# Kernel tuning notes

Measured on AMD Instinct MI355X. Metric: run time of the kernel, lower is better.

The kernel has to match this reference:

```python
import jax, jax.numpy as jnp
import numpy as np

B, DV, W, H = 64, 2048, 14, 14
DQ, DA, G, DH, NC = 2400, 1200, 2, 1200, 3000


def setup_inputs() -> dict:
    key = jax.random.key(0)
    ks = jax.random.split(key, 14)
    s = lambda k, shp, scale=0.02: jax.random.normal(k, shp, dtype=jnp.float32) * scale
    return {
        "input_q": jax.random.normal(ks[0], (B, DQ), dtype=jnp.float32),
        "input_v": jax.random.normal(ks[1], (B, DV, W, H), dtype=jnp.float32),
        "Wv_att": s(ks[2], (DA, DV)),
        "bv_att": s(ks[3], (DA,)),
        "Wq_att": s(ks[4], (DA, DQ)),
        "bq_att": s(ks[5], (DA,)),
        "Watt": s(ks[6], (G, DA)),
        "batt": s(ks[7], (G,)),
        "Wv_fus": s(ks[8], (G, DH, DV)),
        "bv_fus": s(ks[9], (G, DH)),
        "Wq_fus": s(ks[10], (G * DH, DQ)),
        "bq_fus": s(ks[11], (G * DH,)),
        "Wc": s(ks[12], (NC, G * DH)),
        "bc": s(ks[13], (NC,)),
    }


def reference(input_q, input_v, Wv_att, bv_att, Wq_att, bq_att, Watt, batt,
              Wv_fus, bv_fus, Wq_fus, bq_fus, Wc, bc):
    b, dv, w, h = input_v.shape
    n = w * h  # spatial positions

    # --- attention branch (eval mode: dropout = identity) ---
    # 1x1 conv == per-position linear over channels; activation_v = tanh
    xv = jnp.tanh(jnp.einsum('bchw,dc->bdhw', input_v, Wv_att) + bv_att[None, :, None, None])
    xv = xv.reshape(b, -1, n).transpose(0, 2, 1)               # [B, WH, DA]
    # question projection; activation_q = tanh
    xq = jnp.tanh(input_q @ Wq_att.T + bq_att)                 # [B, DA]
    # MLB Hadamard fusion + activation_mm = tanh
    xatt = jnp.tanh(xv * xq[:, None, :])                       # [B, WH, DA]
    # glimpse scores: 1x1 conv over dim_mm channels
    wgt = jnp.einsum('bnd,gd->bgn', xatt, Watt) + batt[None, :, None]  # [B, G, WH]
    att = jax.nn.softmax(wgt, axis=-1)                         # softmax over WH per glimpse

    # weighted sum of ORIGINAL features per glimpse
    v_flat = input_v.reshape(b, dv, n)                         # [B, DV, WH]
    v_att = jnp.einsum('bgn,bdn->bgd', att, v_flat)            # [B, G, DV]

    # --- glimpse fusion + classification ---
    v_fus = jnp.tanh(jnp.einsum('bgd,ghd->bgh', v_att, Wv_fus) + bv_fus)  # [B, G, DH]
    v_fus = v_fus.reshape(b, -1)                               # [B, G*DH] (concat over glimpses)
    q_fus = jnp.tanh(input_q @ Wq_fus.T + bq_fus)              # [B, G*DH]
    x = (v_fus * q_fus) @ Wc.T + bc                            # [B, NC]
    return (x, wgt)
```

## Files before the change

kernel.cpp:

```cpp
#include <hip/hip_runtime.h>
#include <hip/hip_fp16.h>

typedef _Float16 half8 __attribute__((ext_vector_type(8)));
typedef float f32x4 __attribute__((ext_vector_type(4)));

__device__ __forceinline__ float tanh_fast(float x) {
  float e = __expf(2.0f * x);
  return 1.0f - 2.0f / (e + 1.0f);
}

__device__ __forceinline__ void gload16(const _Float16* g, _Float16* l) {
  __builtin_amdgcn_global_load_lds((const __attribute__((address_space(1))) void*)g,
                                   (__attribute__((address_space(3))) void*)l,
                                   16, 0, 0);
}

__global__ __launch_bounds__(256) void k_transpose_v(const float* __restrict__ in,
                                                     _Float16* __restrict__ out) {
  __shared__ float t[64][65];
  int b = blockIdx.z;
  int c0 = blockIdx.y * 64;
  int p0 = blockIdx.x * 64;
  int tid = threadIdx.x;
  int pl = tid & 63;
  #pragma unroll
  for (int s = 0; s < 16; ++s) {
    int cl = (tid >> 6) + s * 4;
    int p = p0 + pl;
    t[cl][pl] = (p < 196) ? in[((size_t)b * 2048 + (c0 + cl)) * 196 + p] : 0.0f;
  }
  __syncthreads();
  int c8 = (tid & 7) * 8;
  #pragma unroll
  for (int s = 0; s < 2; ++s) {
    int p = p0 + (tid >> 3) + s * 32;
    if (p < 196) {
      half8 v;
      #pragma unroll
      for (int j = 0; j < 8; ++j) v[j] = (_Float16)t[c8 + j][(tid >> 3) + s * 32];
      *(half8*)(out + ((size_t)b * 196 + p) * 2048 + c0 + c8) = v;
    }
  }
}

__global__ __launch_bounds__(256) void k_prep(const float* __restrict__ W,
                                              _Float16* __restrict__ Wh,
                                              const float* __restrict__ batt,
                                              float* __restrict__ wgt) {
  int i = blockIdx.x * 256 + threadIdx.x;
  int n = i >> 11;
  Wh[i] = (n < 1200) ? (_Float16)W[i] : (_Float16)0.0f;
  if (i < 25088) wgt[i] = batt[(i / 196) & 1];
}

__global__ __launch_bounds__(256) void k_gemm1(const _Float16* __restrict__ A,
                                               const _Float16* __restrict__ B,
                                               const float* __restrict__ bias,
                                               const float* __restrict__ xq,
                                               const float* __restrict__ Watt,
                                               float* __restrict__ wgt) {
  __shared__ __align__(16) _Float16 As[2][128 * 32];
  __shared__ __align__(16) _Float16 Bs[2][128 * 32];
  int tid = threadIdx.x;
  int n0 = blockIdx.x * 128;
  int m0 = blockIdx.y * 128;
  int lane = tid & 63;
  int wave = tid >> 6;
  int wm = (wave >> 1) * 64;
  int wn = (wave & 1) * 64;
  int fr = lane & 15;
  int fq = lane >> 4;

  int rl = lane >> 2;
  int cch = lane & 3;
  int row0 = wave * 32 + rl;
  int row1 = wave * 32 + 16 + rl;
  int g0 = cch ^ ((row0 >> 1) & 3);
  int g1 = cch ^ ((row1 >> 1) & 3);
  const _Float16* aSrc0 = A + (size_t)(m0 + row0) * 2048 + g0 * 8;
  const _Float16* aSrc1 = A + (size_t)(m0 + row1) * 2048 + g1 * 8;
  const _Float16* bSrc0 = B + (size_t)(n0 + row0) * 2048 + g0 * 8;
  const _Float16* bSrc1 = B + (size_t)(n0 + row1) * 2048 + g1 * 8;

  f32x4 acc[4][4];
  #pragma unroll
  for (int i = 0; i < 4; ++i)
    #pragma unroll
    for (int j = 0; j < 4; ++j) acc[i][j] = (f32x4){0.f, 0.f, 0.f, 0.f};

  auto stage = [&](int buf, int k0) {
    _Float16* dA = &As[buf][(wave * 32) * 32];
    _Float16* dB = &Bs[buf][(wave * 32) * 32];
    gload16(aSrc0 + k0, dA);
    gload16(aSrc1 + k0, dA + 16 * 32);
    gload16(bSrc0 + k0, dB);
    gload16(bSrc1 + k0, dB + 16 * 32);
  };
  int sw = (fr >> 1) & 3;
  auto compute = [&](int buf) {
    half8 af[4], bf[4];
    #pragma unroll
    for (int mt = 0; mt < 4; ++mt)
      af[mt] = *(const half8*)(&As[buf][(wm + mt * 16 + fr) * 32 + ((fq ^ sw) << 3)]);
    #pragma unroll
    for (int nt = 0; nt < 4; ++nt)
      bf[nt] = *(const half8*)(&Bs[buf][(wn + nt * 16 + fr) * 32 + ((fq ^ sw) << 3)]);
    #pragma unroll
    for (int mt = 0; mt < 4; ++mt)
      #pragma unroll
      for (int nt = 0; nt < 4; ++nt)
        acc[mt][nt] = __builtin_amdgcn_mfma_f32_16x16x32_f16(af[mt], bf[nt], acc[mt][nt], 0, 0, 0);
  };

  stage(0, 0);
  stage(1, 32);
  for (int kt = 0; kt < 63; ++kt) {
    int cur = kt & 1;
    asm volatile("s_waitcnt vmcnt(4)" ::: "memory");
    __builtin_amdgcn_s_barrier();
    compute(cur);
    asm volatile("s_waitcnt lgkmcnt(0)" ::: "memory");
    __builtin_amdgcn_s_barrier();
    if (kt < 62) stage(cur, (kt + 2) * 32);
  }
  asm volatile("s_waitcnt vmcnt(0)" ::: "memory");
  __builtin_amdgcn_s_barrier();
  compute(1);

  float s0[16], s1[16];
  #pragma unroll
  for (int i = 0; i < 16; ++i) { s0[i] = 0.f; s1[i] = 0.f; }

  #pragma unroll
  for (int nt = 0; nt < 4; ++nt) {
    int col = n0 + wn + nt * 16 + fr;
    bool ok = col < 1200;
    float bcol = ok ? bias[col] : 0.f;
    float wa0 = ok ? Watt[col] : 0.f;
    float wa1 = ok ? Watt[1200 + col] : 0.f;
    #pragma unroll
    for (int mt = 0; mt < 4; ++mt) {
      #pragma unroll
      for (int r = 0; r < 4; ++r) {
        int row = m0 + wm + mt * 16 + fq * 4 + r;
        int b = row / 196;
        float xqv = ok ? xq[b * 1200 + col] : 0.f;
        float xv = tanh_fast(acc[mt][nt][r] + bcol);
        float xa = tanh_fast(xv * xqv);
        s0[mt * 4 + r] += xa * wa0;
        s1[mt * 4 + r] += xa * wa1;
      }
    }
  }
  #pragma unroll
  for (int i = 0; i < 16; ++i) {
    #pragma unroll
    for (int off = 8; off > 0; off >>= 1) {
      s0[i] += __shfl_down(s0[i], off);
      s1[i] += __shfl_down(s1[i], off);
    }
  }
  if (fr == 0) {
    #pragma unroll
    for (int i = 0; i < 16; ++i) {
      int row = m0 + wm + (i >> 2) * 16 + fq * 4 + (i & 3);
      int b = row / 196;
      int p = row - b * 196;
      atomicAdd(&wgt[(b * 2 + 0) * 196 + p], s0[i]);
      atomicAdd(&wgt[(b * 2 + 1) * 196 + p], s1[i]);
    }
  }
}

__global__ __launch_bounds__(256) void k_vatt(const _Float16* __restrict__ Vt,
                                              const float* __restrict__ wgt,
                                              float* __restrict__ v_att) {
  __shared__ float a0s[196], a1s[196];
  int b = blockIdx.y;
  int tid = threadIdx.x;
  int wv = tid >> 6, lane = tid & 63;
  if (wv < 2) {
    const float* wr = wgt + ((size_t)b * 2 + wv) * 196;
    float v[4];
    #pragma unroll
    for (int i = 0; i < 4; ++i) {
      int n = lane + i * 64;
      v[i] = (n < 196) ? wr[n] : -1e30f;
    }
    float mx = fmaxf(fmaxf(v[0], v[1]), fmaxf(v[2], v[3]));
    #pragma unroll
    for (int off = 32; off > 0; off >>= 1) mx = fmaxf(mx, __shfl_xor(mx, off));
    float s = 0.f;
    #pragma unroll
    for (int i = 0; i < 4; ++i) {
      int n = lane + i * 64;
      float e = (n < 196) ? __expf(v[i] - mx) : 0.f;
      v[i] = e;
      s += e;
    }
    #pragma unroll
    for (int off = 32; off > 0; off >>= 1) s += __shfl_xor(s, off);
    float inv = 1.f / s;
    float* dst = wv ? a1s : a0s;
    #pragma unroll
    for (int i = 0; i < 4; ++i) {
      int n = lane + i * 64;
      if (n < 196) dst[n] = v[i] * inv;
    }
  }
  __syncthreads();
  int d = blockIdx.x * 256 + tid;
  const _Float16* vp = Vt + (size_t)b * 196 * 2048 + d;
  float s0 = 0.f, s1 = 0.f;
  for (int n = 0; n < 196; ++n) {
    float v = (float)vp[(size_t)n * 2048];
    s0 += a0s[n] * v;
    s1 += a1s[n] * v;
  }
  v_att[((size_t)b * 2 + 0) * 2048 + d] = s0;
  v_att[((size_t)b * 2 + 1) * 2048 + d] = s1;
}

__global__ __launch_bounds__(256) void k_skinnyQ(const float* __restrict__ q,
                                                 const float* __restrict__ Wa,
                                                 const float* __restrict__ Wf,
                                                 int S, float* __restrict__ P) {
  __shared__ __align__(16) float As[32][64];
  __shared__ __align__(16) float Ws2[32][64];
  int tid = threadIdx.x;
  int x = blockIdx.x;
  int s = blockIdx.y;
  bool f = x >= 19;
  const float* W = f ? Wf : Wa;
  int nt0 = f ? (x - 19) * 64 : x * 64;
  int N = f ? 2400 : 1200;
  int colBase = f ? 1200 : 0;
  const int K = 2400;
  int tiles = K >> 5;
  int t0 = (s * tiles) / S;
  int t1 = ((s + 1) * tiles) / S;
  int tx = tid & 15, ty = tid >> 4;
  int lm = tid >> 2;
  int lk = (tid & 3) * 8;
  const float* Ab = q + (size_t)lm * K;
  int ng = nt0 + lm;
  const float* Wb = W + (size_t)ng * K;
  bool wok = ng < N;
  float acc[4][4] = {};
  for (int t = t0; t < t1; ++t) {
    int k0 = t * 32;
    __syncthreads();
    #pragma unroll
    for (int j = 0; j < 8; ++j) As[lk + j][lm] = Ab[k0 + lk + j];
    #pragma unroll
    for (int j = 0; j < 8; ++j) Ws2[lk + j][lm] = wok ? Wb[k0 + lk + j] : 0.0f;
    __syncthreads();
    #pragma unroll
    for (int kk = 0; kk < 32; ++kk) {
      f32x4 a = *(const f32x4*)&As[kk][ty * 4];
      f32x4 wv = *(const f32x4*)&Ws2[kk][tx * 4];
      #pragma unroll
      for (int i = 0; i < 4; ++i)
        #pragma unroll
        for (int j = 0; j < 4; ++j) acc[i][j] += a[i] * wv[j];
    }
  }
  #pragma unroll
  for (int i = 0; i < 4; ++i) {
    int m = ty * 4 + i;
    #pragma unroll
    for (int j = 0; j < 4; ++j) {
      int nl = nt0 + tx * 4 + j;
      if (nl < N) P[((size_t)s * 64 + m) * 3600 + colBase + nl] = acc[i][j];
    }
  }
}

__global__ __launch_bounds__(256) void k_combineQ(const float* __restrict__ P, int S,
                                                  const float* __restrict__ bq_att,
                                                  const float* __restrict__ bq_fus,
                                                  float* __restrict__ xq,
                                                  float* __restrict__ q_fus) {
  int i = blockIdx.x * 256 + threadIdx.x;
  if (i >= 230400) return;
  int row = i / 3600, col = i % 3600;
  float sum = 0.f;
  for (int ss = 0; ss < S; ++ss) sum += P[(size_t)ss * 230400 + i];
  if (col < 1200) xq[row * 1200 + col] = tanh_fast(sum + bq_att[col]);
  else            q_fus[row * 2400 + col - 1200] = tanh_fast(sum + bq_fus[col - 1200]);
}

__global__ __launch_bounds__(256) void k_skinny(const float* __restrict__ A1,
                                                const float* __restrict__ A2,
                                                int lda, int strideAz,
                                                const float* __restrict__ W, long strideWz,
                                                int N, int K, int S,
                                                float* __restrict__ P, int ldp, int colOffZ) {
  __shared__ __align__(16) float As[32][64];
  __shared__ __align__(16) float Ws2[32][64];
  int tid = threadIdx.x;
  int z = blockIdx.z;
  int s = blockIdx.y;
  int nt0 = blockIdx.x * 64;
  int tiles = K >> 5;
  int t0 = (s * tiles) / S;
  int t1 = ((s + 1) * tiles) / S;
  int tx = tid & 15, ty = tid >> 4;
  int lm = tid >> 2;
  int lk = (tid & 3) * 8;
  const float* Ab = A1 + (size_t)z * strideAz + (size_t)lm * lda;
  const float* A2b = A2 ? (A2 + (size_t)z * strideAz + (size_t)lm * lda) : nullptr;
  int ng = nt0 + lm;
  const float* Wb = W + (size_t)z * strideWz + (size_t)ng * K;
  bool wok = ng < N;
  float acc[4][4] = {};
  for (int t = t0; t < t1; ++t) {
    int k0 = t * 32;
    __syncthreads();
    #pragma unroll
    for (int j = 0; j < 8; ++j) {
      float v = Ab[k0 + lk + j];
      if (A2b) v *= A2b[k0 + lk + j];
      As[lk + j][lm] = v;
    }
    #pragma unroll
    for (int j = 0; j < 8; ++j) Ws2[lk + j][lm] = wok ? Wb[k0 + lk + j] : 0.0f;
    __syncthreads();
    #pragma unroll
    for (int kk = 0; kk < 32; ++kk) {
      f32x4 a = *(const f32x4*)&As[kk][ty * 4];
      f32x4 wv = *(const f32x4*)&Ws2[kk][tx * 4];
      #pragma unroll
      for (int i = 0; i < 4; ++i)
        #pragma unroll
        for (int j = 0; j < 4; ++j) acc[i][j] += a[i] * wv[j];
    }
  }
  #pragma unroll
  for (int i = 0; i < 4; ++i) {
    int m = ty * 4 + i;
    #pragma unroll
    for (int j = 0; j < 4; ++j) {
      int nl = nt0 + tx * 4 + j;
      if (nl < N) P[((size_t)s * 64 + m) * ldp + z * colOffZ + nl] = acc[i][j];
    }
  }
}

__global__ __launch_bounds__(256) void k_combineVh(const float* __restrict__ P, int S,
                                                   const float* __restrict__ bv_fus,
                                                   const float* __restrict__ q_fus,
                                                   float* __restrict__ h) {
  int i = blockIdx.x * 256 + threadIdx.x;
  if (i >= 153600) return;
  int col = i % 2400;
  float sum = bv_fus[col];
  for (int ss = 0; ss < S; ++ss) sum += P[(size_t)ss * 153600 + i];
  h[i] = tanh_fast(sum) * q_fus[i];
}

__global__ __launch_bounds__(256) void k_combine(const float* __restrict__ P, int S, int ldp,
                                                 const float* __restrict__ bias,
                                                 float* __restrict__ out, int total) {
  int i = blockIdx.x * 256 + threadIdx.x;
  if (i >= total) return;
  float sum = bias[i % ldp];
  for (int ss = 0; ss < S; ++ss) sum += P[(size_t)ss * total + i];
  out[i] = sum;
}

extern "C" void kernel_launch(void* const* d_in, const int* in_sizes, int n_in,
                              void* d_out, int out_size, void* d_ws, size_t ws_size,
                              hipStream_t stream) {
  const float* input_q = (const float*)d_in[0];
  const float* input_v = (const float*)d_in[1];
  const float* Wv_att  = (const float*)d_in[2];
  const float* bv_att  = (const float*)d_in[3];
  const float* Wq_att  = (const float*)d_in[4];
  const float* bq_att  = (const float*)d_in[5];
  const float* Watt    = (const float*)d_in[6];
  const float* batt    = (const float*)d_in[7];
  const float* Wv_fus  = (const float*)d_in[8];
  const float* bv_fus  = (const float*)d_in[9];
  const float* Wq_fus  = (const float*)d_in[10];
  const float* bq_fus  = (const float*)d_in[11];
  const float* Wc      = (const float*)d_in[12];
  const float* bc      = (const float*)d_in[13];
  float* out = (float*)d_out;

  char* ws = (char*)d_ws;
  _Float16* Vt   = (_Float16*)ws; ws += 51380224;
  _Float16* Wh   = (_Float16*)ws; ws += 5242880;
  float* xq      = (float*)ws;    ws += 307200;
  float* v_att   = (float*)ws;    ws += 1048576;
  float* v_fus   = (float*)ws;    ws += 614400;
  float* q_fus   = (float*)ws;    ws += 614400;
  float* P       = (float*)ws;    ws += 14745600;

  float* x_out   = out;
  float* wgt_out = out + 192000;

  const int S = 16;

  k_transpose_v<<<dim3(4, 32, 64), dim3(256), 0, stream>>>(input_v, Vt);
  k_prep<<<dim3(10240), dim3(256), 0, stream>>>(Wv_att, Wh, batt, wgt_out);

  k_skinnyQ<<<dim3(57, S), dim3(256), 0, stream>>>(input_q, Wq_att, Wq_fus, S, P);
  k_combineQ<<<dim3(900), dim3(256), 0, stream>>>(P, S, bq_att, bq_fus, xq, q_fus);

  k_gemm1<<<dim3(10, 98), dim3(256), 0, stream>>>(Vt, Wh, bv_att, xq, Watt, wgt_out);

  k_vatt<<<dim3(8, 64), dim3(256), 0, stream>>>(Vt, wgt_out, v_att);

  k_skinny<<<dim3(19, S, 2), dim3(256), 0, stream>>>(v_att, nullptr, 4096, 2048,
                                                     Wv_fus, 1200L * 2048L, 1200, 2048, S, P, 2400, 1200);
  k_combineVh<<<dim3(600), dim3(256), 0, stream>>>(P, S, bv_fus, q_fus, v_fus);

  k_skinny<<<dim3(47, S, 1), dim3(256), 0, stream>>>(v_fus, nullptr, 2400, 0,
                                                     Wc, 0, 3000, 2400, S, P, 3000, 0);
  k_combine<<<dim3(750), dim3(256), 0, stream>>>(P, S, 3000, bc, x_out, 192000);
}
```

Baseline: 472.1 us.

## Enlarge attention GEMM tiles to 256x256x64 with eight waves

Reworks the fused attention-score GEMM from 128x128x32 tiles with four waves to 256x256x64 tiles with eight waves per block. It uses a new XOR swizzle on the LDS layout, raises MFMA issue priority around the compute bursts, and caches the per-batch xq value in the epilogue. The aim is more data reuse per LDS load and fewer global loads and barriers per FLOP. In exchange it uses about 128 KB of LDS per block, more accumulator registers, and a grid of only 245 blocks, so CU coverage and occupancy drop.

```diff
diff --git a/kernel.cpp b/kernel.cpp
--- a/kernel.cpp
+++ b/kernel.cpp
@@ -53,107 +53,128 @@
   if (i < 25088) wgt[i] = batt[(i / 196) & 1];
 }
 
-__global__ __launch_bounds__(256) void k_gemm1(const _Float16* __restrict__ A,
-                                               const _Float16* __restrict__ B,
-                                               const float* __restrict__ bias,
-                                               const float* __restrict__ xq,
-                                               const float* __restrict__ Watt,
-                                               float* __restrict__ wgt) {
-  __shared__ __align__(16) _Float16 As[2][128 * 32];
-  __shared__ __align__(16) _Float16 Bs[2][128 * 32];
+__global__ __launch_bounds__(512, 2) void k_gemm1(const _Float16* __restrict__ A,
+                                                  const _Float16* __restrict__ B,
+                                                  const float* __restrict__ bias,
+                                                  const float* __restrict__ xq,
+                                                  const float* __restrict__ Watt,
+                                                  float* __restrict__ wgt) {
+  __shared__ __align__(16) _Float16 AS[2][256 * 64];
+  __shared__ __align__(16) _Float16 BS[2][256 * 64];
   int tid = threadIdx.x;
-  int n0 = blockIdx.x * 128;
-  int m0 = blockIdx.y * 128;
+  int n0 = blockIdx.x * 256;
+  int m0 = blockIdx.y * 256;
   int lane = tid & 63;
   int wave = tid >> 6;
-  int wm = (wave >> 1) * 64;
-  int wn = (wave & 1) * 64;
+  int wm = (wave >> 2) * 128;
+  int wn = (wave & 3) * 64;
   int fr = lane & 15;
   int fq = lane >> 4;
 
-  int rl = lane >> 2;
-  int cch = lane & 3;
-  int row0 = wave * 32 + rl;
-  int row1 = wave * 32 + 16 + rl;
-  int g0 = cch ^ ((row0 >> 1) & 3);
-  int g1 = cch ^ ((row1 >> 1) & 3);
-  const _Float16* aSrc0 = A + (size_t)(m0 + row0) * 2048 + g0 * 8;
-  const _Float16* aSrc1 = A + (size_t)(m0 + row1) * 2048 + g1 * 8;
-  const _Float16* bSrc0 = B + (size_t)(n0 + row0) * 2048 + g0 * 8;
-  const _Float16* bSrc1 = B + (size_t)(n0 + row1) * 2048 + g1 * 8;
-
-  f32x4 acc[4][4];
-  #pragma unroll
-  for (int i = 0; i < 4; ++i)
+  const _Float16* ap[4];
+  const _Float16* bp[4];
+  int ldso[4];
+  #pragma unroll
+  for (int i = 0; i < 4; ++i) {
+    int g = i * 512 + tid;
+    int r = g >> 3, c = g & 7;
+    ap[i] = A + (size_t)(m0 + r) * 2048 + ((c ^ (r & 7)) << 3);
+    bp[i] = B + (size_t)(n0 + r) * 2048 + ((c ^ (r & 7)) << 3);
+    ldso[i] = (i * 512 + (tid & ~63)) << 3;
+  }
+
+  f32x4 acc[8][4];
+  #pragma unroll
+  for (int i = 0; i < 8; ++i)
     #pragma unroll
     for (int j = 0; j < 4; ++j) acc[i][j] = (f32x4){0.f, 0.f, 0.f, 0.f};
 
   auto stage = [&](int buf, int k0) {
-    _Float16* dA = &As[buf][(wave * 32) * 32];
-    _Float16* dB = &Bs[buf][(wave * 32) * 32];
-    gload16(aSrc0 + k0, dA);
-    gload16(aSrc1 + k0, dA + 16 * 32);
-    gload16(bSrc0 + k0, dB);
-    gload16(bSrc1 + k0, dB + 16 * 32);
+    #pragma unroll
+    for (int i = 0; i < 4; ++i) gload16(ap[i] + k0, &AS[buf][ldso[i]]);
+    #pragma unroll
+    for (int i = 0; i < 4; ++i) gload16(bp[i] + k0, &BS[buf][ldso[i]]);
   };
-  int sw = (fr >> 1) & 3;
+
   auto compute = [&](int buf) {
-    half8 af[4], bf[4];
-    #pragma unroll
-    for (int mt = 0; mt < 4; ++mt)
-      af[mt] = *(const half8*)(&As[buf][(wm + mt * 16 + fr) * 32 + ((fq ^ sw) << 3)]);
-    #pragma unroll
-    for (int nt = 0; nt < 4; ++nt)
-      bf[nt] = *(const half8*)(&Bs[buf][(wn + nt * 16 + fr) * 32 + ((fq ^ sw) << 3)]);
-    #pragma unroll
-    for (int mt = 0; mt < 4; ++mt)
-      #pragma unroll
-      for (int nt = 0; nt < 4; ++nt)
-        acc[mt][nt] = __builtin_amdgcn_mfma_f32_16x16x32_f16(af[mt], bf[nt], acc[mt][nt], 0, 0, 0);
+    half8 a[4][2], b[2][2];
+    #pragma unroll
+    for (int mh = 0; mh < 2; ++mh) {
+      #pragma unroll
+      for (int mt = 0; mt < 4; ++mt)
+        #pragma unroll
+        for (int kk = 0; kk < 2; ++kk) {
+          int row = wm + mh * 64 + mt * 16 + fr;
+          int c = kk * 4 + fq;
+          a[mt][kk] = *(const half8*)(&AS[buf][row * 64 + ((c ^ (row & 7)) << 3)]);
+        }
+      #pragma unroll
+      for (int nh = 0; nh < 2; ++nh) {
+        #pragma unroll
+        for (int nt = 0; nt < 2; ++nt)
+          #pragma unroll
+          for (int kk = 0; kk < 2; ++kk) {
+            int row = wn + nh * 32 + nt * 16 + fr;
+            int c = kk * 4 + fq;
+            b[nt][kk] = *(const half8*)(&BS[buf][row * 64 + ((c ^ (row & 7)) << 3)]);
+          }
+        __builtin_amdgcn_s_setprio(1);
+        #pragma unroll
+        for (int mt = 0; mt < 4; ++mt)
+          #pragma unroll
+          for (int nt = 0; nt < 2; ++nt)
+            #pragma unroll
+            for (int kk = 0; kk < 2; ++kk)
+              acc[mh * 4 + mt][nh * 2 + nt] = __builtin_amdgcn_mfma_f32_16x16x32_f16(
+                  a[mt][kk], b[nt][kk], acc[mh * 4 + mt][nh * 2 + nt], 0, 0, 0);
+        __builtin_amdgcn_s_setprio(0);
+      }
+    }
   };
 
   stage(0, 0);
-  stage(1, 32);
-  for (int kt = 0; kt < 63; ++kt) {
-    int cur = kt & 1;
-    asm volatile("s_waitcnt vmcnt(4)" ::: "memory");
+  stage(1, 64);
+  for (int t = 0; t < 32; ++t) {
+    int cur = t & 1;
+    if (t < 31) asm volatile("s_waitcnt vmcnt(8)" ::: "memory");
+    else        asm volatile("s_waitcnt vmcnt(0)" ::: "memory");
     __builtin_amdgcn_s_barrier();
+    asm volatile("" ::: "memory");
     compute(cur);
-    asm volatile("s_waitcnt lgkmcnt(0)" ::: "memory");
+    asm volatile("" ::: "memory");
     __builtin_amdgcn_s_barrier();
-    if (kt < 62) stage(cur, (kt + 2) * 32);
-  }
-  asm volatile("s_waitcnt vmcnt(0)" ::: "memory");
-  __builtin_amdgcn_s_barrier();
-  compute(1);
-
-  float s0[16], s1[16];
-  #pragma unroll
-  for (int i = 0; i < 16; ++i) { s0[i] = 0.f; s1[i] = 0.f; }
-
-  #pragma unroll
-  for (int nt = 0; nt < 4; ++nt) {
-    int col = n0 + wn + nt * 16 + fr;
+    if (t < 30) stage(cur, (t + 2) * 64);
+  }
+
+  float s0[32], s1[32];
+  #pragma unroll
+  for (int i = 0; i < 32; ++i) { s0[i] = 0.f; s1[i] = 0.f; }
+
+  #pragma unroll
+  for (int nf = 0; nf < 4; ++nf) {
+    int col = n0 + wn + (nf >> 1) * 32 + (nf & 1) * 16 + fr;
     bool ok = col < 1200;
     float bcol = ok ? bias[col] : 0.f;
     float wa0 = ok ? Watt[col] : 0.f;
     float wa1 = ok ? Watt[1200 + col] : 0.f;
-    #pragma unroll
-    for (int mt = 0; mt < 4; ++mt) {
+    int bprev = -1;
+    float xqv = 0.f;
+    #pragma unroll
+    for (int mf = 0; mf < 8; ++mf) {
       #pragma unroll
       for (int r = 0; r < 4; ++r) {
-        int row = m0 + wm + mt * 16 + fq * 4 + r;
+        int row = m0 + wm + (mf >> 2) * 64 + (mf & 3) * 16 + fq * 4 + r;
         int b = row / 196;
-        float xqv = ok ? xq[b * 1200 + col] : 0.f;
-        float xv = tanh_fast(acc[mt][nt][r] + bcol);
+        if (b != bprev) { bprev = b; xqv = ok ? xq[b * 1200 + col] : 0.f; }
+        float xv = tanh_fast(acc[mf][nf][r] + bcol);
         float xa = tanh_fast(xv * xqv);
-        s0[mt * 4 + r] += xa * wa0;
-        s1[mt * 4 + r] += xa * wa1;
+        s0[mf * 4 + r] += xa * wa0;
+        s1[mf * 4 + r] += xa * wa1;
       }
     }
   }
   #pragma unroll
-  for (int i = 0; i < 16; ++i) {
+  for (int i = 0; i < 32; ++i) {
     #pragma unroll
     for (int off = 8; off > 0; off >>= 1) {
       s0[i] += __shfl_down(s0[i], off);
@@ -162,8 +183,8 @@
   }
   if (fr == 0) {
     #pragma unroll
-    for (int i = 0; i < 16; ++i) {
-      int row = m0 + wm + (i >> 2) * 16 + fq * 4 + (i & 3);
+    for (int i = 0; i < 32; ++i) {
+      int row = m0 + wm + ((i >> 2) >> 2) * 64 + ((i >> 2) & 3) * 16 + fq * 4 + (i & 3);
       int b = row / 196;
       int p = row - b * 196;
       atomicAdd(&wgt[(b * 2 + 0) * 196 + p], s0[i]);
@@ -408,7 +429,7 @@
   k_skinnyQ<<<dim3(57, S), dim3(256), 0, stream>>>(input_q, Wq_att, Wq_fus, S, P);
   k_combineQ<<<dim3(900), dim3(256), 0, stream>>>(P, S, bq_att, bq_fus, xq, q_fus);
 
-  k_gemm1<<<dim3(10, 98), dim3(256), 0, stream>>>(Vt, Wh, bv_att, xq, Watt, wgt_out);
+  k_gemm1<<<dim3(5, 49), dim3(512), 0, stream>>>(Vt, Wh, bv_att, xq, Watt, wgt_out);
 
   k_vatt<<<dim3(8, 64), dim3(256), 0, stream>>>(Vt, wgt_out, v_att);
 
```

Result: slower. 494.1 us (+4.7%).
